# Performance work log

Hardware: AMD Instinct MI355X
Metric: run time of the kernel (lower is better)

Reference implementation:

```python
import jax, jax.numpy as jnp
import numpy as np

NEG_SLOPE = 0.2

def _l2norm(x):
    # F.normalize(x, 2, -1): x / max(||x||_2, 1e-12)
    return x / jnp.maximum(jnp.linalg.norm(x, axis=-1, keepdims=True), 1e-12)

def _segment_softmax(e, dst, n_dst):
    m = jax.ops.segment_max(e, dst, num_segments=n_dst)
    m = jnp.where(jnp.isfinite(m), m, 0.0)
    ex = jnp.exp(e - m[dst])
    denom = jax.ops.segment_sum(ex, dst, num_segments=n_dst)
    return ex / (denom[dst] + 1e-16)

def _gat_conv(x_src, x_dst, edge_index, W, a_src, a_dst, b, n_dst):
    # PyG GATConv, heads=1, concat, shared lin for src/dst (int in_channels)
    h_src = x_src @ W                      # [Ns, H]
    h_dst = x_dst @ W                      # [Nd, H]
    src, dst = edge_index[0], edge_index[1]
    al_s = h_src @ a_src                   # [Ns]
    al_d = h_dst @ a_dst                   # [Nd]
    e = jax.nn.leaky_relu(al_s[src] + al_d[dst], NEG_SLOPE)  # [E]
    coef = _segment_softmax(e, dst, n_dst)                   # [E]
    out = jax.ops.segment_sum(coef[:, None] * h_src[src], dst, num_segments=n_dst)
    return out + b

def setup_inputs() -> dict:
    key = jax.random.key(0)
    ks = jax.random.split(key, 32)
    nd, npr, nc, H, L, B = 2000, 19000, 100, 256, 2, 8192
    E_pp, E_dp, E_cp = 400000, 60000, 300000
    s = 0.1
    inp = {
        'drug_emb': jax.random.normal(ks[0], (nd, H), jnp.float32),
        'protein_emb': jax.random.normal(ks[1], (npr, H), jnp.float32),
        'cell_emb': jax.random.normal(ks[2], (nc, H), jnp.float32),
        'W_pp': jax.random.normal(ks[3], (L, H, H), jnp.float32) * s,
        'as_pp': jax.random.normal(ks[4], (L, H), jnp.float32) * s,
        'ad_pp': jax.random.normal(ks[5], (L, H), jnp.float32) * s,
        'b_pp': jax.random.normal(ks[6], (L, H), jnp.float32) * s,
        'W_dp': jax.random.normal(ks[7], (L, H, H), jnp.float32) * s,
        'as_dp': jax.random.normal(ks[8], (L, H), jnp.float32) * s,
        'ad_dp': jax.random.normal(ks[9], (L, H), jnp.float32) * s,
        'b_dp': jax.random.normal(ks[10], (L, H), jnp.float32) * s,
        'W_cp': jax.random.normal(ks[11], (L, H, H), jnp.float32) * s,
        'as_cp': jax.random.normal(ks[12], (L, H), jnp.float32) * s,
        'ad_cp': jax.random.normal(ks[13], (L, H), jnp.float32) * s,
        'b_cp': jax.random.normal(ks[14], (L, H), jnp.float32) * s,
        'W1': jax.random.normal(ks[15], (3 * H, 6 * H), jnp.float32) * s,
        'b1': jax.random.normal(ks[16], (6 * H,), jnp.float32) * s,
        'W2': jax.random.normal(ks[17], (6 * H, 2 * H), jnp.float32) * s,
        'b2': jax.random.normal(ks[18], (2 * H,), jnp.float32) * s,
        'W3': jax.random.normal(ks[19], (2 * H, 2), jnp.float32) * s,
        'b3': jax.random.normal(ks[20], (2,), jnp.float32) * s,
        'edge_pp': jnp.stack([jax.random.randint(ks[21], (E_pp,), 0, npr),
                              jax.random.randint(ks[22], (E_pp,), 0, npr)]),
        'edge_dp': jnp.stack([jax.random.randint(ks[23], (E_dp,), 0, npr),
                              jax.random.randint(ks[24], (E_dp,), 0, nd)]),
        'edge_cp': jnp.stack([jax.random.randint(ks[25], (E_cp,), 0, npr),
                              jax.random.randint(ks[26], (E_cp,), 0, nc)]),
        'drug1': jax.random.randint(ks[27], (B,), 0, nd),
        'drug2': jax.random.randint(ks[28], (B,), 0, nd),
        'cell': jax.random.randint(ks[29], (B,), 0, nc),
    }
    return inp

def reference(drug_emb, protein_emb, cell_emb,
              W_pp, as_pp, ad_pp, b_pp,
              W_dp, as_dp, ad_dp, b_dp,
              W_cp, as_cp, ad_cp, b_cp,
              W1, b1, W2, b2, W3, b3,
              edge_pp, edge_dp, edge_cp, drug1, drug2, cell):
    n_drug, n_prot, n_cell = drug_emb.shape[0], protein_emb.shape[0], cell_emb.shape[0]
    num_layer = W_pp.shape[0]
    # node ids are arange -> embedding lookup is the full table
    x_d, x_p, x_c = drug_emb, protein_emb, cell_emb
    # p-p GATConv adds self loops (default add_self_loops=True)
    loop = jnp.arange(n_prot, dtype=edge_pp.dtype)
    ei_pp = jnp.concatenate([edge_pp, jnp.stack([loop, loop])], axis=1)
    for l in range(num_layer):
        x_p = _gat_conv(x_p, x_p, ei_pp, W_pp[l], as_pp[l], ad_pp[l], b_pp[l], n_prot)
        x_p = _l2norm(x_p)
        x_d = jax.nn.relu(_gat_conv(x_p, x_d, edge_dp, W_dp[l], as_dp[l], ad_dp[l], b_dp[l], n_drug))
        x_c = jax.nn.relu(_gat_conv(x_p, x_c, edge_cp, W_cp[l], as_cp[l], ad_cp[l], b_cp[l], n_cell))
    hid = jnp.concatenate([_l2norm(x_d[drug1]), _l2norm(x_d[drug2]), _l2norm(x_c[cell])], axis=1)
    h = jax.nn.relu(hid @ W1 + b1)
    h = jax.nn.relu(h @ W2 + b2)
    logits = h @ W3 + b3
    return logits
```

## Files before the change

### kernel.cpp

```cpp
#include <hip/hip_runtime.h>
#include <hip/hip_bf16.h>

#define HDIM 256
#define NEG_SLOPE 0.2f
#define NB 128
#define SLICES 8
#define TBN 64
#define TBK 32
#define PITCH 40

typedef __attribute__((ext_vector_type(8))) short bf16x8;
typedef __attribute__((ext_vector_type(4))) float f32x4;

__device__ inline uint f2pl(float x) {
  __hip_bfloat16 h = __float2bfloat16(x);
  ushort hi = *(ushort*)&h;
  float r = x - __bfloat162float(h);
  __hip_bfloat16 l = __float2bfloat16(r);
  ushort lo = *(ushort*)&l;
  return (uint)hi | ((uint)lo << 16);
}
__device__ inline ushort f2b(float x) {
  __hip_bfloat16 h = __float2bfloat16(x);
  return *(ushort*)&h;
}
__device__ inline float b2f(ushort u) {
  uint x = ((uint)u) << 16;
  return __int_as_float((int)x);
}

static inline int cdiv(int a, int b) { return (a + b - 1) / b; }

__global__ void fillf_kernel(float* __restrict__ p, float v, int n) {
  int i = blockIdx.x * blockDim.x + threadIdx.x;
  if (i < n) p[i] = v;
}

__global__ void wconv_split_kernel(const float* __restrict__ W,
                                   ushort* __restrict__ WTh, ushort* __restrict__ WTl,
                                   int K, int N) {
  int i = blockIdx.x * 256 + threadIdx.x;
  if (i >= K * N) return;
  int k = i / N, n = i - k * N;
  uint p = f2pl(W[i]);
  WTh[(size_t)n * K + k] = (ushort)(p & 0xffff);
  WTl[(size_t)n * K + k] = (ushort)(p >> 16);
}

__global__ void f32_to_b16_kernel(const float* __restrict__ in, ushort* __restrict__ out, int n) {
  int i = blockIdx.x * 256 + threadIdx.x;
  if (i < n) out[i] = f2b(in[i]);
}

__global__ void f32_to_split_kernel(const float* __restrict__ in,
                                    ushort* __restrict__ oh, ushort* __restrict__ ol, int n) {
  int i = blockIdx.x * 256 + threadIdx.x;
  if (i >= n) return;
  uint p = f2pl(in[i]);
  oh[i] = (ushort)(p & 0xffff);
  ol[i] = (ushort)(p >> 16);
}

__global__ __launch_bounds__(256) void matvec_all_kernel(
    const float* __restrict__ Wpp, const float* __restrict__ aspp, const float* __restrict__ adpp,
    const float* __restrict__ Wdp, const float* __restrict__ asdp, const float* __restrict__ addp,
    const float* __restrict__ Wcp, const float* __restrict__ ascp, const float* __restrict__ adcp,
    float* __restrict__ wv) {
  int b = blockIdx.x;
  int l = b / 6, r = b - l * 6, type = r >> 1, isd = r & 1;
  const float* W = (type == 0 ? Wpp : type == 1 ? Wdp : Wcp) + (size_t)l * HDIM * HDIM;
  const float* a = (type == 0 ? (isd ? adpp : aspp)
                  : type == 1 ? (isd ? addp : asdp)
                              : (isd ? adcp : ascp)) + (size_t)l * HDIM;
  int k = threadIdx.x;
  const float4* Wr = (const float4*)(W + (size_t)k * HDIM);
  float s = 0.f;
#pragma unroll 8
  for (int n4 = 0; n4 < HDIM / 4; ++n4) {
    float4 w = Wr[n4];
    float4 av = *(const float4*)(a + n4 * 4);
    s += w.x * av.x + w.y * av.y + w.z * av.z + w.w * av.w;
  }
  wv[(size_t)b * HDIM + k] = s;
}

__global__ __launch_bounds__(256) void combine_h1_kernel(
    const float* __restrict__ P1, const float* __restrict__ P2, const float* __restrict__ P3,
    const int* __restrict__ g1, const int* __restrict__ g2, const int* __restrict__ g3,
    int row0, ushort* __restrict__ h1h, ushort* __restrict__ h1l, int M, int K) {
  int t = blockIdx.x * 256 + threadIdx.x;
  int kq = K >> 2;
  if (t >= M * kq) return;
  int row = t / kq, c4 = t - row * kq;
  int bi = row0 + row;
  size_t o = (size_t)c4 * 4;
  float4 a = *(const float4*)(P1 + (size_t)g1[bi] * K + o);
  float4 b = *(const float4*)(P2 + (size_t)g2[bi] * K + o);
  float4 c = *(const float4*)(P3 + (size_t)g3[bi] * K + o);
  uint p0 = f2pl(fmaxf(a.x + b.x + c.x, 0.f));
  uint p1 = f2pl(fmaxf(a.y + b.y + c.y, 0.f));
  uint p2 = f2pl(fmaxf(a.z + b.z + c.z, 0.f));
  uint p3 = f2pl(fmaxf(a.w + b.w + c.w, 0.f));
  ushort4 h = {(ushort)(p0 & 0xffff), (ushort)(p1 & 0xffff), (ushort)(p2 & 0xffff), (ushort)(p3 & 0xffff)};
  ushort4 l = {(ushort)(p0 >> 16), (ushort)(p1 >> 16), (ushort)(p2 >> 16), (ushort)(p3 >> 16)};
  *(ushort4*)(h1h + (size_t)row * K + o) = h;
  *(ushort4*)(h1l + (size_t)row * K + o) = l;
}

template <int TBM_, int ACT>
__global__ __launch_bounds__(256) void mfma_gemm(
    const ushort* __restrict__ Ahg, const ushort* __restrict__ Alg,
    const ushort* __restrict__ Bhg, const ushort* __restrict__ Blg,
    int ldb, const float* __restrict__ bias,
    float* __restrict__ C, int M, int N, int K) {
  __shared__ __align__(16) ushort Ah[2][TBM_][PITCH];
  __shared__ __align__(16) ushort Al[2][TBM_][PITCH];
  __shared__ __align__(16) ushort Bh[2][TBN][PITCH];
  __shared__ __align__(16) ushort Bl[2][TBN][PITCH];

  constexpr int NU = TBM_ / 64;
  constexpr int TM = TBM_ / 32;

  const int tid = threadIdx.x;
  const int lane = tid & 63;
  const int wid = tid >> 6;
  const int wm = wid & 1, wn = wid >> 1;
  const int l16 = lane & 15;
  const int quad = lane >> 4;
  const int m0 = blockIdx.x * TBM_;
  const int n0 = blockIdx.y * TBN;

  const int co = (lane & 3) * 8;
  const int r4 = lane >> 2;

  uint4 rah[NU], ral[NU], rbh, rbl;

  auto LOADA = [&](int k0) {
#pragma unroll
    for (int u = 0; u < NU; ++u) {
      int r = wid * (TBM_ / 4) + r4 + 16 * u;
      int gm = m0 + r;
      if (gm < M) {
        size_t o = (size_t)gm * K + k0 + co;
        rah[u] = *(const uint4*)(Ahg + o);
        ral[u] = *(const uint4*)(Alg + o);
      } else {
        rah[u] = make_uint4(0, 0, 0, 0);
        ral[u] = make_uint4(0, 0, 0, 0);
      }
    }
    {
      int r = wid * 16 + r4;
      size_t o = (size_t)(n0 + r) * ldb + k0 + co;
      rbh = *(const uint4*)(Bhg + o);
      rbl = *(const uint4*)(Blg + o);
    }
  };
  auto STORE = [&](int b) {
#pragma unroll
    for (int u = 0; u < NU; ++u) {
      int r = wid * (TBM_ / 4) + r4 + 16 * u;
      *(uint4*)&Ah[b][r][co] = rah[u];
      *(uint4*)&Al[b][r][co] = ral[u];
    }
    int r = wid * 16 + r4;
    *(uint4*)&Bh[b][r][co] = rbh;
    *(uint4*)&Bl[b][r][co] = rbl;
  };

  f32x4 acc[TM][2];
#pragma unroll
  for (int i = 0; i < TM; ++i)
#pragma unroll
    for (int j = 0; j < 2; ++j) acc[i][j] = (f32x4){0.f, 0.f, 0.f, 0.f};

  auto COMPUTE = [&](int b) {
    bf16x8 ahf[TM], alf[TM], bhf[2], blf[2];
#pragma unroll
    for (int t = 0; t < TM; ++t) {
      int r = wm * (TBM_ / 2) + t * 16 + l16;
      ahf[t] = *(const bf16x8*)&Ah[b][r][quad * 8];
      alf[t] = *(const bf16x8*)&Al[b][r][quad * 8];
    }
#pragma unroll
    for (int t = 0; t < 2; ++t) {
      int r = wn * 32 + t * 16 + l16;
      bhf[t] = *(const bf16x8*)&Bh[b][r][quad * 8];
      blf[t] = *(const bf16x8*)&Bl[b][r][quad * 8];
    }
#pragma unroll
    for (int tm = 0; tm < TM; ++tm)
#pragma unroll
      for (int tn = 0; tn < 2; ++tn) {
        acc[tm][tn] = __builtin_amdgcn_mfma_f32_16x16x32_bf16(ahf[tm], bhf[tn], acc[tm][tn], 0, 0, 0);
        acc[tm][tn] = __builtin_amdgcn_mfma_f32_16x16x32_bf16(ahf[tm], blf[tn], acc[tm][tn], 0, 0, 0);
        acc[tm][tn] = __builtin_amdgcn_mfma_f32_16x16x32_bf16(alf[tm], bhf[tn], acc[tm][tn], 0, 0, 0);
      }
  };

  LOADA(0);
  STORE(0);
  int cur = 0;
  for (int k0 = TBK; k0 < K; k0 += TBK) {
    LOADA(k0);
    __syncthreads();
    COMPUTE(cur);
    STORE(cur ^ 1);
    cur ^= 1;
  }
  __syncthreads();
  COMPUTE(cur);

#pragma unroll
  for (int tn = 0; tn < 2; ++tn) {
    int col = n0 + wn * 32 + tn * 16 + l16;
    float bv = bias ? bias[col] : 0.f;
#pragma unroll
    for (int tm = 0; tm < TM; ++tm) {
#pragma unroll
      for (int r = 0; r < 4; ++r) {
        int row = m0 + wm * (TBM_ / 2) + tm * 16 + quad * 4 + r;
        if (row >= M) continue;
        float v = acc[tm][tn][r] + bv;
        if (ACT == 1) v = fmaxf(v, 0.f);
        C[(size_t)row * N + col] = v;
      }
    }
  }
}

template <int TBM_, int ACT>
static void gemm_launch(hipStream_t s,
                        const ushort* Ahg, const ushort* Alg,
                        const ushort* Bhg, const ushort* Blg,
                        int ldb, const float* bias, float* C,
                        int M, int N, int K) {
  dim3 g(cdiv(M, TBM_), N / TBN);
  mfma_gemm<TBM_, ACT><<<g, 256, 0, s>>>(Ahg, Alg, Bhg, Blg, ldb, bias, C, M, N, K);
}

__global__ __launch_bounds__(256) void rowdot_kernel(
    const float* __restrict__ H, const float* __restrict__ a,
    float* __restrict__ out, int n) {
  int row = blockIdx.x * 4 + (threadIdx.x >> 6);
  if (row >= n) return;
  int lane = threadIdx.x & 63;
  const float* h = H + (size_t)row * HDIM;
  float s = 0.f;
#pragma unroll
  for (int u = 0; u < 4; ++u) {
    int c = lane + u * 64;
    s += h[c] * a[c];
  }
#pragma unroll
  for (int off = 32; off; off >>= 1) s += __shfl_down(s, off);
  if (lane == 0) out[row] = s;
}

__global__ __launch_bounds__(256) void rowdot2_kernel(
    const float* __restrict__ H, const float* __restrict__ a1, const float* __restrict__ a2,
    float* __restrict__ o1, float* __restrict__ o2, int n) {
  int row = blockIdx.x * 4 + (threadIdx.x >> 6);
  if (row >= n) return;
  int lane = threadIdx.x & 63;
  const float* h = H + (size_t)row * HDIM;
  float s1 = 0.f, s2 = 0.f;
#pragma unroll
  for (int u = 0; u < 4; ++u) {
    int c = lane + u * 64;
    float hv = h[c];
    s1 += hv * a1[c];
    s2 += hv * a2[c];
  }
#pragma unroll
  for (int off = 32; off; off >>= 1) {
    s1 += __shfl_down(s1, off);
    s2 += __shfl_down(s2, off);
  }
  if (lane == 0) { o1[row] = s1; o2[row] = s2; }
}

__global__ __launch_bounds__(256) void hist_kernel(
    const int* __restrict__ src, const int* __restrict__ dst, int E, int nloops,
    int Nd, int* __restrict__ offs) {
  extern __shared__ int bins[];
  int tot = E + nloops;
  int chunk = (tot + NB - 1) / NB;
  int b = blockIdx.x;
  int s0 = b * chunk, s1 = min(s0 + chunk, tot);
  for (int i = threadIdx.x; i < Nd; i += 256) bins[i] = 0;
  __syncthreads();
  for (int i = s0 + threadIdx.x; i < s1; i += 256) {
    int d = (i < E) ? dst[i] : (i - E);
    atomicAdd(&bins[d], 1);
  }
  __syncthreads();
  for (int i = threadIdx.x; i < Nd; i += 256) offs[(size_t)i * NB + b] = bins[i];
}

__global__ __launch_bounds__(256) void scan_bins_kernel(
    int* __restrict__ offs, int* __restrict__ binsum, int Nd) {
  int d = blockIdx.x * 4 + (threadIdx.x >> 6);
  if (d >= Nd) return;
  int lane = threadIdx.x & 63;
  int* p = offs + (size_t)d * NB;
  int v0 = p[2 * lane], v1 = p[2 * lane + 1];
  int s = v0 + v1;
  int t = s;
#pragma unroll
  for (int o = 1; o < 64; o <<= 1) { int u = __shfl_up(t, o); if (lane >= o) t += u; }
  int excl = t - s;
  p[2 * lane] = excl;
  p[2 * lane + 1] = excl + v0;
  if (lane == 63) binsum[d] = t;
}

__global__ __launch_bounds__(256) void scan_base_kernel(
    const int* __restrict__ binsum, int* __restrict__ rowptr, int Nd) {
  __shared__ int wsum[4];
  __shared__ int carry;
  if (threadIdx.x == 0) carry = 0;
  __syncthreads();
  int lane = threadIdx.x & 63, w = threadIdx.x >> 6;
  for (int t0 = 0; t0 < Nd; t0 += 256) {
    int i = t0 + threadIdx.x;
    int v = (i < Nd) ? binsum[i] : 0;
    int t = v;
#pragma unroll
    for (int o = 1; o < 64; o <<= 1) { int u = __shfl_up(t, o); if (lane >= o) t += u; }
    if (lane == 63) wsum[w] = t;
    __syncthreads();
    int add = carry;
    for (int k = 0; k < w; ++k) add += wsum[k];
    if (i < Nd) rowptr[i] = t - v + add;
    __syncthreads();
    if (threadIdx.x == 0) carry += wsum[0] + wsum[1] + wsum[2] + wsum[3];
    __syncthreads();
  }
  if (threadIdx.x == 0) rowptr[Nd] = carry;
}

__global__ __launch_bounds__(256) void scatter_kernel(
    const int* __restrict__ src, const int* __restrict__ dst, int E, int nloops,
    int Nd, const int* __restrict__ offs, const int* __restrict__ rowptr,
    uint* __restrict__ sd) {
  extern __shared__ int bins[];
  int tot = E + nloops;
  int chunk = (tot + NB - 1) / NB;
  int b = blockIdx.x;
  int s0 = b * chunk, s1 = min(s0 + chunk, tot);
  for (int i = threadIdx.x; i < Nd; i += 256) bins[i] = 0;
  __syncthreads();
  for (int i = s0 + threadIdx.x; i < s1; i += 256) {
    int s_, d_;
    if (i < E) { s_ = src[i]; d_ = dst[i]; }
    else       { s_ = d_ = i - E; }
    int local = atomicAdd(&bins[d_], 1);
    int pos = rowptr[d_] + offs[(size_t)d_ * NB + b] + local;
    sd[pos] = (uint)s_ | ((uint)d_ << 16);
  }
}

__global__ __launch_bounds__(256) void gat_agg_split(
    const int* __restrict__ rowptr, const uint* __restrict__ sd,
    const float* __restrict__ als, const float* __restrict__ ald,
    const ushort* __restrict__ Xb,
    ushort* __restrict__ aggh, ushort* __restrict__ aggl, int n) {
  int d = blockIdx.x * 4 + (threadIdx.x >> 6);
  if (d >= n) return;
  int lane = threadIdx.x & 63;
  int r0 = rowptr[d], r1 = rowptr[d + 1];
  float aldd = ald[d];
  float dsum = 0.f;
  for (int j = r0 + lane; j < r1; j += 64) {
    float e = als[sd[j] & 0xffff] + aldd;
    e = (e > 0.f) ? e : NEG_SLOPE * e;
    dsum += __expf(e);
  }
#pragma unroll
  for (int o = 32; o; o >>= 1) dsum += __shfl_xor(dsum, o);
  float rden = 1.f / (dsum + 1e-16f);

  float4 acc = make_float4(0.f, 0.f, 0.f, 0.f);
  for (int b = r0; b < r1; b += 64) {
    int j = b + lane;
    float exv = 0.f; int srcv = 0;
    if (j < r1) {
      uint p = sd[j];
      srcv = p & 0xffff;
      float e = als[srcv] + aldd;
      e = (e > 0.f) ? e : NEG_SLOPE * e;
      exv = __expf(e) * rden;
    }
    int cnt = min(64, r1 - b);
    for (int t0 = 0; t0 < cnt; t0 += 8) {
      float cf[8]; int sv[8];
#pragma unroll
      for (int u = 0; u < 8; ++u) {
        cf[u] = __shfl(exv, t0 + u);
        sv[u] = __shfl(srcv, t0 + u);
      }
      ushort4 hv[8];
#pragma unroll
      for (int u = 0; u < 8; ++u)
        hv[u] = *(const ushort4*)(Xb + (size_t)sv[u] * HDIM + lane * 4);
#pragma unroll
      for (int u = 0; u < 8; ++u) {
        acc.x += cf[u] * b2f(hv[u].x);
        acc.y += cf[u] * b2f(hv[u].y);
        acc.z += cf[u] * b2f(hv[u].z);
        acc.w += cf[u] * b2f(hv[u].w);
      }
    }
  }
  uint p0 = f2pl(acc.x), p1 = f2pl(acc.y), p2 = f2pl(acc.z), p3 = f2pl(acc.w);
  ushort4 h = {(ushort)(p0 & 0xffff), (ushort)(p1 & 0xffff), (ushort)(p2 & 0xffff), (ushort)(p3 & 0xffff)};
  ushort4 l = {(ushort)(p0 >> 16), (ushort)(p1 >> 16), (ushort)(p2 >> 16), (ushort)(p3 >> 16)};
  *(ushort4*)(aggh + (size_t)d * HDIM + lane * 4) = h;
  *(ushort4*)(aggl + (size_t)d * HDIM + lane * 4) = l;
}

__global__ __launch_bounds__(256) void gat_agg_slice(
    const int* __restrict__ rowptr, const uint* __restrict__ sd,
    const float* __restrict__ als, const float* __restrict__ ald,
    const ushort* __restrict__ Xb, float* __restrict__ out32, int n) {
  int d = blockIdx.x / SLICES;
  int sl = blockIdx.x - d * SLICES;
  if (d >= n) return;
  int lane = threadIdx.x & 63, w = threadIdx.x >> 6;
  int r0 = rowptr[d], r1 = rowptr[d + 1];
  float aldd = ald[d];
  float dsum = 0.f;
  for (int j = r0 + threadIdx.x; j < r1; j += 256) {
    float e = als[sd[j] & 0xffff] + aldd;
    e = (e > 0.f) ? e : NEG_SLOPE * e;
    dsum += __expf(e);
  }
#pragma unroll
  for (int o = 32; o; o >>= 1) dsum += __shfl_xor(dsum, o);
  __shared__ float wd[4];
  if (lane == 0) wd[w] = dsum;
  __syncthreads();
  float rden = 1.f / (wd[0] + wd[1] + wd[2] + wd[3] + 1e-16f);
  int deg = r1 - r0;
  int per_b = (deg + SLICES - 1) / SLICES;
  int b0 = r0 + sl * per_b, b1 = min(b0 + per_b, r1);
  int wdeg = b1 - b0;
  if (wdeg <= 0) return;
  int per_w = (wdeg + 3) >> 2;
  int w0 = b0 + w * per_w, w1 = min(w0 + per_w, b1);

  float4 acc = make_float4(0.f, 0.f, 0.f, 0.f);
  for (int b = w0; b < w1; b += 64) {
    int j = b + lane;
    float exv = 0.f; int srcv = 0;
    if (j < w1) {
      uint p = sd[j];
      srcv = p & 0xffff;
      float e = als[srcv] + aldd;
      e = (e > 0.f) ? e : NEG_SLOPE * e;
      exv = __expf(e) * rden;
    }
    int cnt = min(64, w1 - b);
    for (int t0 = 0; t0 < cnt; t0 += 8) {
      float cf[8]; int sv[8];
#pragma unroll
      for (int u = 0; u < 8; ++u) {
        cf[u] = __shfl(exv, t0 + u);
        sv[u] = __shfl(srcv, t0 + u);
      }
      ushort4 hv[8];
#pragma unroll
      for (int u = 0; u < 8; ++u)
        hv[u] = *(const ushort4*)(Xb + (size_t)sv[u] * HDIM + lane * 4);
#pragma unroll
      for (int u = 0; u < 8; ++u) {
        acc.x += cf[u] * b2f(hv[u].x);
        acc.y += cf[u] * b2f(hv[u].y);
        acc.z += cf[u] * b2f(hv[u].z);
        acc.w += cf[u] * b2f(hv[u].w);
      }
    }
  }
  float* o = out32 + (size_t)d * HDIM + lane * 4;
  atomicAdd(o + 0, acc.x); atomicAdd(o + 1, acc.y);
  atomicAdd(o + 2, acc.z); atomicAdd(o + 3, acc.w);
}

__global__ __launch_bounds__(256) void l2norm_f32b_kernel(
    const float* __restrict__ in, float* __restrict__ outf, ushort* __restrict__ outb, int n) {
  int row = blockIdx.x * 4 + (threadIdx.x >> 6);
  if (row >= n) return;
  int lane = threadIdx.x & 63;
  float v[4];
  float ss = 0.f;
#pragma unroll
  for (int u = 0; u < 4; ++u) {
    float t = in[(size_t)row * HDIM + lane + u * 64];
    v[u] = t; ss += t * t;
  }
#pragma unroll
  for (int off = 32; off; off >>= 1) ss += __shfl_xor(ss, off);
  float sc = 1.0f / fmaxf(sqrtf(ss), 1e-12f);
#pragma unroll
  for (int u = 0; u < 4; ++u) {
    float f = v[u] * sc;
    int c = lane + u * 64;
    outf[(size_t)row * HDIM + c] = f;
    outb[(size_t)row * HDIM + c] = f2b(f);
  }
}

__global__ __launch_bounds__(256) void l2norm_split_kernel(
    const float* __restrict__ in,
    ushort* __restrict__ oh, ushort* __restrict__ ol, int n) {
  int row = blockIdx.x * 4 + (threadIdx.x >> 6);
  if (row >= n) return;
  int lane = threadIdx.x & 63;
  float v[4];
  float ss = 0.f;
#pragma unroll
  for (int u = 0; u < 4; ++u) {
    int c = lane + u * 64;
    float t = in[(size_t)row * HDIM + c];
    v[u] = t;
    ss += t * t;
  }
#pragma unroll
  for (int off = 32; off; off >>= 1) ss += __shfl_xor(ss, off);
  float sc = 1.0f / fmaxf(sqrtf(ss), 1e-12f);
#pragma unroll
  for (int u = 0; u < 4; ++u) {
    int c = lane + u * 64;
    uint p = f2pl(v[u] * sc);
    oh[(size_t)row * HDIM + c] = (ushort)(p & 0xffff);
    ol[(size_t)row * HDIM + c] = (ushort)(p >> 16);
  }
}

__global__ __launch_bounds__(256) void head3_kernel(
    const float* __restrict__ h2, const float* __restrict__ W3, const float* __restrict__ b3,
    float* __restrict__ out, int M, int K) {
  int i = blockIdx.x * 4 + (threadIdx.x >> 6);
  int lane = threadIdx.x & 63;
  if (i >= M) return;
  float s0 = 0.f, s1 = 0.f;
  for (int k = lane; k < K; k += 64) {
    float h = h2[(size_t)i * K + k];
    s0 += h * W3[k * 2 + 0];
    s1 += h * W3[k * 2 + 1];
  }
#pragma unroll
  for (int off = 32; off; off >>= 1) {
    s0 += __shfl_down(s0, off);
    s1 += __shfl_down(s1, off);
  }
  if (lane == 0) {
    out[(size_t)i * 2 + 0] = s0 + b3[0];
    out[(size_t)i * 2 + 1] = s1 + b3[1];
  }
}

static void build_sorted(hipStream_t stream,
                         const int* src, const int* dst, int E, int nloops, int Nd,
                         int* offs, int* binsum, int* rowptr, uint* sd) {
  size_t lds = (size_t)Nd * sizeof(int);
  hist_kernel<<<NB, 256, lds, stream>>>(src, dst, E, nloops, Nd, offs);
  scan_bins_kernel<<<cdiv(Nd, 4), 256, 0, stream>>>(offs, binsum, Nd);
  scan_base_kernel<<<1, 256, 0, stream>>>(binsum, rowptr, Nd);
  scatter_kernel<<<NB, 256, lds, stream>>>(src, dst, E, nloops, Nd, offs, rowptr, sd);
}

extern "C" void kernel_launch(void* const* d_in, const int* in_sizes, int n_in,
                              void* d_out, int out_size, void* d_ws, size_t ws_size,
                              hipStream_t stream) {
  const float* drug_emb = (const float*)d_in[0];
  const float* prot_emb = (const float*)d_in[1];
  const float* cell_emb = (const float*)d_in[2];
  const float* W_pp = (const float*)d_in[3];
  const float* as_pp = (const float*)d_in[4];
  const float* ad_pp = (const float*)d_in[5];
  const float* b_pp = (const float*)d_in[6];
  const float* W_dp = (const float*)d_in[7];
  const float* as_dp = (const float*)d_in[8];
  const float* ad_dp = (const float*)d_in[9];
  const float* b_dp = (const float*)d_in[10];
  const float* W_cp = (const float*)d_in[11];
  const float* as_cp = (const float*)d_in[12];
  const float* ad_cp = (const float*)d_in[13];
  const float* b_cp = (const float*)d_in[14];
  const float* W1 = (const float*)d_in[15];
  const float* b1 = (const float*)d_in[16];
  const float* W2 = (const float*)d_in[17];
  const float* b2 = (const float*)d_in[18];
  const float* W3 = (const float*)d_in[19];
  const float* b3 = (const float*)d_in[20];
  const int* edge_pp = (const int*)d_in[21];
  const int* edge_dp = (const int*)d_in[22];
  const int* edge_cp = (const int*)d_in[23];
  const int* drug1 = (const int*)d_in[24];
  const int* drug2 = (const int*)d_in[25];
  const int* cellb = (const int*)d_in[26];

  const int ND = in_sizes[0] / HDIM;
  const int NP = in_sizes[1] / HDIM;
  const int NC = in_sizes[2] / HDIM;
  const int L = in_sizes[3] / (HDIM * HDIM);
  const int E_pp = in_sizes[21] / 2;
  const int E_dp = in_sizes[22] / 2;
  const int E_cp = in_sizes[23] / 2;
  const int B = in_sizes[24];
  (void)n_in; (void)out_size;

  const int* src_pp = edge_pp;          const int* dst_pp = edge_pp + E_pp;
  const int* src_dp = edge_dp;          const int* dst_dp = edge_dp + E_dp;
  const int* src_cp = edge_cp;          const int* dst_cp = edge_cp + E_cp;
  const int tot_pp = E_pp + NP, tot_dp = E_dp, tot_cp = E_cp;
  int maxN = NP > ND ? NP : ND; if (NC > maxN) maxN = NC;

  char* wsb = (char*)d_ws;
  size_t off = 0;
  auto alloc = [&](size_t bytes) -> void* {
    void* p = wsb + off;
    off += (bytes + 255) & ~(size_t)255;
    return p;
  };

  float* Xp  = (float*)alloc((size_t)NP * HDIM * 4);
  ushort* Xpb = (ushort*)alloc((size_t)NP * HDIM * 2);
  float* Xd  = (float*)alloc((size_t)ND * HDIM * 4);
  float* Xc  = (float*)alloc((size_t)NC * HDIM * 4);
  ushort* xdnh = (ushort*)alloc((size_t)ND * HDIM * 2);
  ushort* xdnl = (ushort*)alloc((size_t)ND * HDIM * 2);
  ushort* xcnh = (ushort*)alloc((size_t)NC * HDIM * 2);
  ushort* xcnl = (ushort*)alloc((size_t)NC * HDIM * 2);
  ushort* WTpph = (ushort*)alloc((size_t)L * HDIM * HDIM * 2);
  ushort* WTppl = (ushort*)alloc((size_t)L * HDIM * HDIM * 2);
  ushort* WTdph = (ushort*)alloc((size_t)L * HDIM * HDIM * 2);
  ushort* WTdpl = (ushort*)alloc((size_t)L * HDIM * HDIM * 2);
  ushort* WTcph = (ushort*)alloc((size_t)L * HDIM * HDIM * 2);
  ushort* WTcpl = (ushort*)alloc((size_t)L * HDIM * HDIM * 2);
  ushort* cth = (ushort*)alloc((size_t)NC * HDIM * 2);
  ushort* ctl = (ushort*)alloc((size_t)NC * HDIM * 2);
  float* wv  = (float*)alloc((size_t)L * 6 * HDIM * 4);
  float* als1 = (float*)alloc((size_t)maxN * 4);
  float* als2 = (float*)alloc((size_t)maxN * 4);
  float* ald1 = (float*)alloc((size_t)maxN * 4);
  float* ald2 = (float*)alloc((size_t)maxN * 4);
  int* binsum = (int*)alloc((size_t)maxN * 4);
  int* rp_pp = (int*)alloc((size_t)(NP + 1) * 4);
  int* rp_dp = (int*)alloc((size_t)(ND + 1) * 4);
  int* rp_cp = (int*)alloc((size_t)(NC + 1) * 4);
  uint* sd_pp = (uint*)alloc((size_t)tot_pp * 4);
  uint* sd_dp = (uint*)alloc((size_t)tot_dp * 4);
  uint* sd_cp = (uint*)alloc((size_t)tot_cp * 4);
  float* out32 = (float*)alloc((size_t)NC * HDIM * 4);
  size_t S0 = off;

  int* offs = (int*)(wsb + S0);
  build_sorted(stream, src_pp, dst_pp, E_pp, NP, NP, offs, binsum, rp_pp, sd_pp);
  build_sorted(stream, src_dp, dst_dp, E_dp, 0, ND, offs, binsum, rp_dp, sd_dp);
  build_sorted(stream, src_cp, dst_cp, E_cp, 0, NC, offs, binsum, rp_cp, sd_cp);

  for (int l = 0; l < L; ++l) {
    int WOFF = l * HDIM * HDIM;
    wconv_split_kernel<<<cdiv(HDIM * HDIM, 256), 256, 0, stream>>>(W_pp + WOFF, WTpph + WOFF, WTppl + WOFF, HDIM, HDIM);
    wconv_split_kernel<<<cdiv(HDIM * HDIM, 256), 256, 0, stream>>>(W_dp + WOFF, WTdph + WOFF, WTdpl + WOFF, HDIM, HDIM);
    wconv_split_kernel<<<cdiv(HDIM * HDIM, 256), 256, 0, stream>>>(W_cp + WOFF, WTcph + WOFF, WTcpl + WOFF, HDIM, HDIM);
  }
  matvec_all_kernel<<<L * 6, 256, 0, stream>>>(W_pp, as_pp, ad_pp, W_dp, as_dp, ad_dp,
                                               W_cp, as_cp, ad_cp, wv);
  f32_to_b16_kernel<<<cdiv(NP * HDIM, 256), 256, 0, stream>>>(prot_emb, Xpb, NP * HDIM);

  size_t aggB = ((size_t)NP * HDIM * 2 + 255) & ~(size_t)255;
  ushort* aggh = (ushort*)(wsb + S0);
  ushort* aggl = (ushort*)(wsb + S0 + aggB);
  float* tmp = (float*)(wsb + S0 + 2 * aggB);

  for (int l = 0; l < L; ++l) {
    const int WOFF = l * HDIM * HDIM, VOFF = l * HDIM;
    const float* wvl = wv + (size_t)l * 6 * HDIM;
    const float* Xp_cur = (l == 0) ? prot_emb : Xp;
    const float* Xd_cur = (l == 0) ? drug_emb : Xd;
    const float* Xc_cur = (l == 0) ? cell_emb : Xc;

    rowdot2_kernel<<<cdiv(NP, 4), 256, 0, stream>>>(Xp_cur, wvl + 0 * HDIM, wvl + 1 * HDIM,
                                                    als1, ald1, NP);
    gat_agg_split<<<cdiv(NP, 4), 256, 0, stream>>>(rp_pp, sd_pp, als1, ald1, Xpb, aggh, aggl, NP);
    gemm_launch<128, 0>(stream, aggh, aggl, WTpph + WOFF, WTppl + WOFF, HDIM,
                        b_pp + VOFF, tmp, NP, HDIM, HDIM);
    l2norm_f32b_kernel<<<cdiv(NP, 4), 256, 0, stream>>>(tmp, Xp, Xpb, NP);

    rowdot2_kernel<<<cdiv(NP, 4), 256, 0, stream>>>(Xp, wvl + 2 * HDIM, wvl + 4 * HDIM,
                                                    als1, als2, NP);
    rowdot_kernel<<<cdiv(ND, 4), 256, 0, stream>>>(Xd_cur, wvl + 3 * HDIM, ald1, ND);
    rowdot_kernel<<<cdiv(NC, 4), 256, 0, stream>>>(Xc_cur, wvl + 5 * HDIM, ald2, NC);

    gat_agg_split<<<cdiv(ND, 4), 256, 0, stream>>>(rp_dp, sd_dp, als1, ald1, Xpb, aggh, aggl, ND);
    gemm_launch<64, 1>(stream, aggh, aggl, WTdph + WOFF, WTdpl + WOFF, HDIM,
                       b_dp + VOFF, Xd, ND, HDIM, HDIM);

    fillf_kernel<<<cdiv(NC * HDIM, 256), 256, 0, stream>>>(out32, 0.f, NC * HDIM);
    gat_agg_slice<<<NC * SLICES, 256, 0, stream>>>(rp_cp, sd_cp, als2, ald2, Xpb, out32, NC);
    f32_to_split_kernel<<<cdiv(NC * HDIM, 256), 256, 0, stream>>>(out32, cth, ctl, NC * HDIM);
    gemm_launch<64, 1>(stream, cth, ctl, WTcph + WOFF, WTcpl + WOFF, HDIM,
                       b_cp + VOFF, Xc, NC, HDIM, HDIM);
  }

  l2norm_split_kernel<<<cdiv(ND, 4), 256, 0, stream>>>(Xd, xdnh, xdnl, ND);
  l2norm_split_kernel<<<cdiv(NC, 4), 256, 0, stream>>>(Xc, xcnh, xcnl, NC);

  const int N1 = 6 * HDIM;
  const int N2 = 2 * HDIM;
  const int K1 = 3 * HDIM;
  ushort* W1Th = (ushort*)(wsb + S0);
  ushort* W1Tl = W1Th + (size_t)N1 * K1;
  ushort* W2Th = W1Tl + (size_t)N1 * K1;
  ushort* W2Tl = W2Th + (size_t)N2 * N1;
  float* P1 = (float*)(W2Tl + (size_t)N2 * N1);
  float* P2 = P1 + (size_t)ND * N1;
  float* P3 = P2 + (size_t)ND * N1;
  ushort* h1h = (ushort*)(P3 + (size_t)NC * N1);
  size_t wsz = ws_size ? ws_size : ((size_t)1 << 30);
  size_t fixed = S0 + ((size_t)N1 * K1 + (size_t)N2 * N1) * 4
               + ((size_t)(2 * ND + NC) * N1) * 4;
  int CH = 8192;
  while (CH > 1024 && fixed + (size_t)CH * (N1 * 4 + N2 * 4) > wsz) CH >>= 1;
  ushort* h1l = h1h + (size_t)CH * N1;
  float* h2 = (float*)(h1l + (size_t)CH * N1);

  wconv_split_kernel<<<cdiv(K1 * N1, 256), 256, 0, stream>>>(W1, W1Th, W1Tl, K1, N1);
  wconv_split_kernel<<<cdiv(N1 * N2, 256), 256, 0, stream>>>(W2, W2Th, W2Tl, N1, N2);

  gemm_launch<64, 0>(stream, xdnh, xdnl, W1Th, W1Tl, K1, nullptr, P1, ND, N1, HDIM);
  gemm_launch<64, 0>(stream, xdnh, xdnl, W1Th + HDIM, W1Tl + HDIM, K1, nullptr, P2, ND, N1, HDIM);
  gemm_launch<64, 0>(stream, xcnh, xcnl, W1Th + 2 * HDIM, W1Tl + 2 * HDIM, K1, b1, P3, NC, N1, HDIM);

  float* outp = (float*)d_out;
  for (int c0 = 0; c0 < B; c0 += CH) {
    int M = (B - c0) < CH ? (B - c0) : CH;
    combine_h1_kernel<<<cdiv(M * (N1 / 4), 256), 256, 0, stream>>>(
        P1, P2, P3, drug1, drug2, cellb, c0, h1h, h1l, M, N1);
    gemm_launch<128, 1>(stream, h1h, h1l, W2Th, W2Tl, N1, b2, h2, M, N2, N1);
    head3_kernel<<<cdiv(M, 4), 256, 0, stream>>>(h2, W3, b3, outp + (size_t)c0 * 2, M, N2);
  }
}
```

Baseline: 739.2 us.

## Fuse attention row-dots into l2norm, merge weight conversions, double-register GEMM prefetch

The protein attention dot products for the current layer and the next layer are now computed inside the l2norm kernel, which removes two full passes over the 19000x256 protein features per layer. The six weight-split launches are merged into one kernel. The GEMM main loop now keeps two register sets for prefetch so that global loads for the next tile are issued before compute on the current one. The cost is higher register pressure in the GEMM, and the new loop assumes K/TBK is even and at least 2.

```diff
diff --git a/kernel.cpp b/kernel.cpp
--- a/kernel.cpp
+++ b/kernel.cpp
@@ -45,6 +45,26 @@
   uint p = f2pl(W[i]);
   WTh[(size_t)n * K + k] = (ushort)(p & 0xffff);
   WTl[(size_t)n * K + k] = (ushort)(p >> 16);
+}
+
+__global__ void wconv_split3_kernel(
+    const float* __restrict__ Wpp, const float* __restrict__ Wdp, const float* __restrict__ Wcp,
+    ushort* __restrict__ WTpph, ushort* __restrict__ WTppl,
+    ushort* __restrict__ WTdph, ushort* __restrict__ WTdpl,
+    ushort* __restrict__ WTcph, ushort* __restrict__ WTcpl, int L) {
+  const int per = HDIM * HDIM;
+  int i = blockIdx.x * 256 + threadIdx.x;
+  if (i >= 3 * L * per) return;
+  int mat = i / per;
+  int r = i - mat * per;
+  int l = mat / 3, ty = mat - l * 3;
+  const float* W = (ty == 0 ? Wpp : ty == 1 ? Wdp : Wcp) + (size_t)l * per;
+  ushort* Th = (ty == 0 ? WTpph : ty == 1 ? WTdph : WTcph) + (size_t)l * per;
+  ushort* Tl = (ty == 0 ? WTppl : ty == 1 ? WTdpl : WTcpl) + (size_t)l * per;
+  int k = r >> 8, n = r & (HDIM - 1);
+  uint p = f2pl(W[r]);
+  Th[(size_t)n * HDIM + k] = (ushort)(p & 0xffff);
+  Tl[(size_t)n * HDIM + k] = (ushort)(p >> 16);
 }
 
 __global__ void f32_to_b16_kernel(const float* __restrict__ in, ushort* __restrict__ out, int n) {
@@ -133,9 +153,10 @@
   const int co = (lane & 3) * 8;
   const int r4 = lane >> 2;
 
-  uint4 rah[NU], ral[NU], rbh, rbl;
-
-  auto LOADA = [&](int k0) {
+  uint4 rah0[NU], ral0[NU], rbh0, rbl0;
+  uint4 rah1[NU], ral1[NU], rbh1, rbl1;
+
+  auto LOADA = [&](uint4* rah, uint4* ral, uint4& rbh, uint4& rbl, int k0) {
 #pragma unroll
     for (int u = 0; u < NU; ++u) {
       int r = wid * (TBM_ / 4) + r4 + 16 * u;
@@ -156,7 +177,7 @@
       rbl = *(const uint4*)(Blg + o);
     }
   };
-  auto STORE = [&](int b) {
+  auto STORE = [&](const uint4* rah, const uint4* ral, const uint4& rbh, const uint4& rbl, int b) {
 #pragma unroll
     for (int u = 0; u < NU; ++u) {
       int r = wid * (TBM_ / 4) + r4 + 16 * u;
@@ -198,18 +219,28 @@
       }
   };
 
-  LOADA(0);
-  STORE(0);
-  int cur = 0;
-  for (int k0 = TBK; k0 < K; k0 += TBK) {
-    LOADA(k0);
+  const int NK = K / TBK;
+  LOADA(rah0, ral0, rbh0, rbl0, 0);
+  LOADA(rah1, ral1, rbh1, rbl1, TBK);
+  STORE(rah0, ral0, rbh0, rbl0, 0);
+  int k = 2 * TBK;
+  for (int t = 0; t < (NK - 2) / 2; ++t) {
     __syncthreads();
-    COMPUTE(cur);
-    STORE(cur ^ 1);
-    cur ^= 1;
+    LOADA(rah0, ral0, rbh0, rbl0, k);
+    COMPUTE(0);
+    STORE(rah1, ral1, rbh1, rbl1, 1);
+    k += TBK;
+    __syncthreads();
+    LOADA(rah1, ral1, rbh1, rbl1, k);
+    COMPUTE(1);
+    STORE(rah0, ral0, rbh0, rbl0, 0);
+    k += TBK;
   }
   __syncthreads();
-  COMPUTE(cur);
+  COMPUTE(0);
+  STORE(rah1, ral1, rbh1, rbl1, 1);
+  __syncthreads();
+  COMPUTE(1);
 
 #pragma unroll
   for (int tn = 0; tn < 2; ++tn) {
@@ -487,8 +518,12 @@
   atomicAdd(o + 2, acc.z); atomicAdd(o + 3, acc.w);
 }
 
-__global__ __launch_bounds__(256) void l2norm_f32b_kernel(
-    const float* __restrict__ in, float* __restrict__ outf, ushort* __restrict__ outb, int n) {
+__global__ __launch_bounds__(256) void l2norm_f32b_dots_kernel(
+    const float* __restrict__ in, float* __restrict__ outf, ushort* __restrict__ outb,
+    const float* __restrict__ v1, const float* __restrict__ v2,
+    const float* __restrict__ v3, const float* __restrict__ v4,
+    float* __restrict__ o1, float* __restrict__ o2,
+    float* __restrict__ o3, float* __restrict__ o4, int n) {
   int row = blockIdx.x * 4 + (threadIdx.x >> 6);
   if (row >= n) return;
   int lane = threadIdx.x & 63;
@@ -502,12 +537,26 @@
 #pragma unroll
   for (int off = 32; off; off >>= 1) ss += __shfl_xor(ss, off);
   float sc = 1.0f / fmaxf(sqrtf(ss), 1e-12f);
+  float d1 = 0.f, d2 = 0.f, d3 = 0.f, d4 = 0.f;
 #pragma unroll
   for (int u = 0; u < 4; ++u) {
     float f = v[u] * sc;
     int c = lane + u * 64;
     outf[(size_t)row * HDIM + c] = f;
     outb[(size_t)row * HDIM + c] = f2b(f);
+    d1 += f * v1[c];
+    d2 += f * v2[c];
+    if (o3) { d3 += f * v3[c]; d4 += f * v4[c]; }
+  }
+#pragma unroll
+  for (int off = 32; off; off >>= 1) {
+    d1 += __shfl_xor(d1, off);
+    d2 += __shfl_xor(d2, off);
+    if (o3) { d3 += __shfl_xor(d3, off); d4 += __shfl_xor(d4, off); }
+  }
+  if (lane == 0) {
+    o1[row] = d1; o2[row] = d2;
+    if (o3) { o3[row] = d3; o4[row] = d4; }
   }
 }
 
@@ -643,6 +692,8 @@
   ushort* cth = (ushort*)alloc((size_t)NC * HDIM * 2);
   ushort* ctl = (ushort*)alloc((size_t)NC * HDIM * 2);
   float* wv  = (float*)alloc((size_t)L * 6 * HDIM * 4);
+  float* pals = (float*)alloc((size_t)maxN * 4);
+  float* pald = (float*)alloc((size_t)maxN * 4);
   float* als1 = (float*)alloc((size_t)maxN * 4);
   float* als2 = (float*)alloc((size_t)maxN * 4);
   float* ald1 = (float*)alloc((size_t)maxN * 4);
@@ -662,12 +713,8 @@
   build_sorted(stream, src_dp, dst_dp, E_dp, 0, ND, offs, binsum, rp_dp, sd_dp);
   build_sorted(stream, src_cp, dst_cp, E_cp, 0, NC, offs, binsum, rp_cp, sd_cp);
 
-  for (int l = 0; l < L; ++l) {
-    int WOFF = l * HDIM * HDIM;
-    wconv_split_kernel<<<cdiv(HDIM * HDIM, 256), 256, 0, stream>>>(W_pp + WOFF, WTpph + WOFF, WTppl + WOFF, HDIM, HDIM);
-    wconv_split_kernel<<<cdiv(HDIM * HDIM, 256), 256, 0, stream>>>(W_dp + WOFF, WTdph + WOFF, WTdpl + WOFF, HDIM, HDIM);
-    wconv_split_kernel<<<cdiv(HDIM * HDIM, 256), 256, 0, stream>>>(W_cp + WOFF, WTcph + WOFF, WTcpl + WOFF, HDIM, HDIM);
-  }
+  wconv_split3_kernel<<<cdiv(3 * L * HDIM * HDIM, 256), 256, 0, stream>>>(
+      W_pp, W_dp, W_cp, WTpph, WTppl, WTdph, WTdpl, WTcph, WTcpl, L);
   matvec_all_kernel<<<L * 6, 256, 0, stream>>>(W_pp, as_pp, ad_pp, W_dp, as_dp, ad_dp,
                                                W_cp, as_cp, ad_cp, wv);
   f32_to_b16_kernel<<<cdiv(NP * HDIM, 256), 256, 0, stream>>>(prot_emb, Xpb, NP * HDIM);
@@ -677,22 +724,26 @@
   ushort* aggl = (ushort*)(wsb + S0 + aggB);
   float* tmp = (float*)(wsb + S0 + 2 * aggB);
 
+  rowdot2_kernel<<<cdiv(NP, 4), 256, 0, stream>>>(prot_emb, wv + 0 * HDIM, wv + 1 * HDIM,
+                                                  pals, pald, NP);
+
   for (int l = 0; l < L; ++l) {
     const int WOFF = l * HDIM * HDIM, VOFF = l * HDIM;
     const float* wvl = wv + (size_t)l * 6 * HDIM;
-    const float* Xp_cur = (l == 0) ? prot_emb : Xp;
+    const float* wvn = wv + (size_t)(l + 1) * 6 * HDIM;
     const float* Xd_cur = (l == 0) ? drug_emb : Xd;
     const float* Xc_cur = (l == 0) ? cell_emb : Xc;
-
-    rowdot2_kernel<<<cdiv(NP, 4), 256, 0, stream>>>(Xp_cur, wvl + 0 * HDIM, wvl + 1 * HDIM,
-                                                    als1, ald1, NP);
-    gat_agg_split<<<cdiv(NP, 4), 256, 0, stream>>>(rp_pp, sd_pp, als1, ald1, Xpb, aggh, aggl, NP);
+    bool last = (l == L - 1);
+
+    gat_agg_split<<<cdiv(NP, 4), 256, 0, stream>>>(rp_pp, sd_pp, pals, pald, Xpb, aggh, aggl, NP);
     gemm_launch<128, 0>(stream, aggh, aggl, WTpph + WOFF, WTppl + WOFF, HDIM,
                         b_pp + VOFF, tmp, NP, HDIM, HDIM);
-    l2norm_f32b_kernel<<<cdiv(NP, 4), 256, 0, stream>>>(tmp, Xp, Xpb, NP);
-
-    rowdot2_kernel<<<cdiv(NP, 4), 256, 0, stream>>>(Xp, wvl + 2 * HDIM, wvl + 4 * HDIM,
-                                                    als1, als2, NP);
+    l2norm_f32b_dots_kernel<<<cdiv(NP, 4), 256, 0, stream>>>(
+        tmp, Xp, Xpb,
+        wvl + 2 * HDIM, wvl + 4 * HDIM,
+        last ? nullptr : (wvn + 0 * HDIM), last ? nullptr : (wvn + 1 * HDIM),
+        als1, als2, last ? nullptr : pals, last ? nullptr : pald, NP);
+
     rowdot_kernel<<<cdiv(ND, 4), 256, 0, stream>>>(Xd_cur, wvl + 3 * HDIM, ald1, ND);
     rowdot_kernel<<<cdiv(NC, 4), 256, 0, stream>>>(Xc_cur, wvl + 5 * HDIM, ald2, NC);
 
```

After: 717.6 us. 2.9% less time.
